# Performance work log

Measured on AMD Instinct MI355X. Metric: run time of the kernel, lower is better.

The kernel has to match this reference:

```python
import jax, jax.numpy as jnp
import numpy as np

N, E, FN, FE, H, L, S = 50000, 800000, 16, 8, 64, 3, 32

def layernorm(h, g, b, eps=1e-5):
    mu = h.mean(-1, keepdims=True)
    var = ((h - mu) ** 2).mean(-1, keepdims=True)
    return (h - mu) / jnp.sqrt(var + eps) * g + b

def setup_inputs() -> dict:
    key = jax.random.key(0)
    ks = iter(jax.random.split(key, 64))
    nrm = lambda shape: jax.random.normal(next(ks), shape, jnp.float32) * 0.05
    inp = {}
    inp['x'] = jax.random.normal(next(ks), (N, FN), jnp.float32)
    inp['edge_index'] = jax.random.randint(next(ks), (2, E), 0, N)
    inp['edge_attr'] = jax.random.normal(next(ks), (E, FE), jnp.float32)
    # node / edge encoders: Linear -> ReLU -> LayerNorm
    inp['Wn'] = nrm((FN, H)); inp['bn'] = jnp.zeros((H,)); inp['gn'] = jnp.ones((H,)); inp['betan'] = jnp.zeros((H,))
    inp['We'] = nrm((FE, H)); inp['be'] = jnp.zeros((H,)); inp['ge'] = jnp.ones((H,)); inp['betae'] = jnp.zeros((H,))
    # EdgeConv MLPs (stacked over layers): Linear(2H,H) -> ReLU -> Linear(H,H)
    inp['Wc1'] = nrm((L, 2 * H, H)); inp['bc1'] = jnp.zeros((L, H))
    inp['Wc2'] = nrm((L, H, H)); inp['bc2'] = jnp.zeros((L, H))
    # GATConv (heads=1): lin weight, att_src, att_dst, bias
    inp['Wg'] = nrm((L, H, H)); inp['att_src'] = nrm((L, H)); inp['att_dst'] = nrm((L, H)); inp['bg'] = jnp.zeros((L, H))
    # q predictor
    inp['Wq1'] = nrm((H, H)); inp['bq1'] = jnp.zeros((H,)); inp['gq'] = jnp.ones((H,)); inp['betaq'] = jnp.zeros((H,))
    inp['Wq2'] = nrm((H, S)); inp['bq2'] = jnp.zeros((S,))
    # value predictor
    inp['Wv1'] = nrm((H, H)); inp['bv1'] = jnp.zeros((H,)); inp['gv'] = jnp.ones((H,)); inp['betav'] = jnp.zeros((H,))
    inp['Wv2'] = nrm((H, 1)); inp['bv2'] = jnp.zeros((1,))
    return inp

def reference(x, edge_index, edge_attr, Wn, bn, gn, betan, We, be, ge, betae,
              Wc1, bc1, Wc2, bc2, Wg, att_src, att_dst, bg,
              Wq1, bq1, gq, betaq, Wq2, bq2, Wv1, bv1, gv, betav, Wv2, bv2):
    n = x.shape[0]
    src, dst = edge_index[0], edge_index[1]  # PyG: row=source(j), col=target(i)
    h = layernorm(jax.nn.relu(x @ Wn + bn), gn, betan)
    _ea = layernorm(jax.nn.relu(edge_attr @ We + be), ge, betae)  # encoded but unused by EdgeConv message (faithful)
    loop = jnp.arange(n)
    gsrc = jnp.concatenate([src, loop])  # GAT adds self-loops
    gdst = jnp.concatenate([dst, loop])
    for l in range(L):
        # EdgeConv: gather x_i (target), x_j (source), concat, MLP, scatter-max at target
        m = jnp.concatenate([h[dst], h[src]], axis=1)  # [E, 2H]
        m = jax.nn.relu(m @ Wc1[l] + bc1[l]) @ Wc2[l] + bc2[l]
        agg = jax.ops.segment_max(m, dst, num_segments=n)
        agg = jnp.where(jnp.isneginf(agg), 0.0, agg)  # PyG scatter-max leaves empty rows at 0
        # GATConv (1 head): alpha = softmax_i(leaky_relu(a_s.xg_j + a_d.xg_i))
        xg = h @ Wg[l]
        a_s = xg @ att_src[l]
        a_d = xg @ att_dst[l]
        e = jax.nn.leaky_relu(a_s[gsrc] + a_d[gdst], 0.2)
        emax = jax.ops.segment_max(e, gdst, num_segments=n)
        w = jnp.exp(e - emax[gdst])
        alpha = w / jax.ops.segment_sum(w, gdst, num_segments=n)[gdst]
        att = jax.ops.segment_sum(xg[gsrc] * alpha[:, None], gdst, num_segments=n) + bg[l]
        h = jax.nn.relu(h + agg + att)
    t = h[0]
    tq = layernorm(jax.nn.relu(t @ Wq1 + bq1), gq, betaq)
    q_values = tq @ Wq2 + bq2
    tv = layernorm(jax.nn.relu(t @ Wv1 + bv1), gv, betav)
    value = tv @ Wv2 + bv2
    return (q_values, value)
```

## Files before the change

### kernel.cpp

```cpp
#include <hip/hip_runtime.h>
#include <math.h>

#define N_NODES 50000
#define N_EDGES 800000
#define FN_DIM 16
#define HD 64
#define T_CAP 8192
#define T2_CAP 512
#define MAXDEG 128

__device__ __forceinline__ float wsum64(float v) {
    #pragma unroll
    for (int o = 1; o < 64; o <<= 1) v += __shfl_xor(v, o);
    return v;
}
__device__ __forceinline__ float wmax64(float v) {
    #pragma unroll
    for (int o = 1; o < 64; o <<= 1) v = fmaxf(v, __shfl_xor(v, o));
    return v;
}
__device__ __forceinline__ float lrelu02(float v) { return v > 0.f ? v : 0.2f * v; }

__global__ void k_mark2(const int* __restrict__ ei, int* need1, int* need2) {
    int e = blockIdx.x * blockDim.x + threadIdx.x;
    if (e == 0) { need1[0] = 1; need2[0] = 1; }
    if (e >= N_EDGES) return;
    if (ei[N_EDGES + e] == 0) { int s = ei[e]; need2[s] = 1; need1[s] = 1; }
}
__global__ void k_mark1(const int* __restrict__ ei, const int* __restrict__ need2, int* need1) {
    int e = blockIdx.x * blockDim.x + threadIdx.x;
    if (e >= N_EDGES) return;
    if (need2[ei[N_EDGES + e]]) need1[ei[e]] = 1;
}
__global__ void k_compact(const int* __restrict__ need1, const int* __restrict__ need2,
                          int* list1, int* list2, int* idx1, int* idx2, int* cnt) {
    int i = blockIdx.x * blockDim.x + threadIdx.x;
    if (i >= N_NODES) return;
    if (need1[i]) { int p = atomicAdd(&cnt[0], 1); if (p < T_CAP)  { list1[p] = i; idx1[i] = p; } }
    if (need2[i]) { int p = atomicAdd(&cnt[1], 1); if (p < T2_CAP) { list2[p] = i; idx2[i] = p; } }
}
__global__ void k_bucket(const int* __restrict__ ei, const int* __restrict__ need1,
                         const int* __restrict__ need2,
                         const int* __restrict__ idx1, const int* __restrict__ idx2,
                         int* eb1, int* deg1, int* eb2, int* deg2, int* eb3, int* deg3) {
    int e = blockIdx.x * blockDim.x + threadIdx.x;
    if (e >= N_EDGES) return;
    int d = ei[N_EDGES + e];
    int s = ei[e];
    if (need1[d]) {
        int t = idx1[d];
        if ((unsigned)t < T_CAP) { int p = atomicAdd(&deg1[t], 1); if (p < MAXDEG) eb1[t * MAXDEG + p] = s; }
    }
    if (need2[d]) {
        int t = idx2[d];
        if ((unsigned)t < T2_CAP) { int p = atomicAdd(&deg2[t], 1); if (p < MAXDEG) eb2[t * MAXDEG + p] = s; }
    }
    if (d == 0) { int p = atomicAdd(deg3, 1); if (p < MAXDEG) eb3[p] = s; }
}

template<int LM>
__device__ __forceinline__ float node_h(int i, int lane,
    const float* __restrict__ x, const float* __restrict__ Wn, const float* __restrict__ bn,
    const float* __restrict__ gn, const float* __restrict__ betan,
    const float* __restrict__ hin) {
    if (LM == 0) {
        float acc = bn[lane];
        #pragma unroll
        for (int k = 0; k < FN_DIM; k++) acc += x[i * FN_DIM + k] * Wn[k * HD + lane];
        float v = fmaxf(acc, 0.f);
        float mu = wsum64(v) * (1.f / 64.f);
        float d = v - mu;
        float var = wsum64(d * d) * (1.f / 64.f);
        return d * rsqrtf(var + 1e-5f) * gn[lane] + betan[lane];
    } else {
        return hin[i * HD + lane];
    }
}

__device__ __forceinline__ void heads_eval(float hv, int lane,
    const float* __restrict__ Wq1, const float* __restrict__ bq1,
    const float* __restrict__ gq, const float* __restrict__ betaq,
    const float* __restrict__ Wq2, const float* __restrict__ bq2,
    const float* __restrict__ Wv1, const float* __restrict__ bv1,
    const float* __restrict__ gv, const float* __restrict__ betav,
    const float* __restrict__ Wv2, const float* __restrict__ bv2,
    float* __restrict__ out) {
    float acc = bq1[lane];
    #pragma unroll 8
    for (int k = 0; k < 64; k++) acc += __shfl(hv, k) * Wq1[k * 64 + lane];
    float r = fmaxf(acc, 0.f);
    float mu = wsum64(r) * (1.f / 64.f);
    float d = r - mu;
    float var = wsum64(d * d) * (1.f / 64.f);
    float tq = d * rsqrtf(var + 1e-5f) * gq[lane] + betaq[lane];
    float accv = bv1[lane];
    #pragma unroll 8
    for (int k = 0; k < 64; k++) accv += __shfl(hv, k) * Wv1[k * 64 + lane];
    float rv = fmaxf(accv, 0.f);
    float muv = wsum64(rv) * (1.f / 64.f);
    float dv = rv - muv;
    float varv = wsum64(dv * dv) * (1.f / 64.f);
    float tv = dv * rsqrtf(varv + 1e-5f) * gv[lane] + betav[lane];
    int s = lane & 31;
    float q = bq2[s];
    #pragma unroll 8
    for (int k = 0; k < 64; k++) q += __shfl(tq, k) * Wq2[k * 32 + s];
    if (lane < 32) out[lane] = q;
    float vsum = wsum64(tv * Wv2[lane]);
    if (lane == 0) out[32] = vsum + bv2[0];
}

template<int LM>
__global__ __launch_bounds__(256) void k_layer(
    const float* __restrict__ x, const float* __restrict__ Wn, const float* __restrict__ bn,
    const float* __restrict__ gn, const float* __restrict__ betan,
    const float* __restrict__ hin,
    const float* __restrict__ Wc1, const float* __restrict__ bc1,
    const float* __restrict__ Wc2, const float* __restrict__ bc2,
    const float* __restrict__ Wg, const float* __restrict__ atts, const float* __restrict__ attd,
    const float* __restrict__ bgv,
    const int* __restrict__ tlist, const int* __restrict__ cntp, int tcap,
    const int* __restrict__ eb, const int* __restrict__ deg,
    float* __restrict__ hout,
    const float* __restrict__ Wq1, const float* __restrict__ bq1,
    const float* __restrict__ gq, const float* __restrict__ betaq,
    const float* __restrict__ Wq2, const float* __restrict__ bq2,
    const float* __restrict__ Wv1, const float* __restrict__ bv1,
    const float* __restrict__ gv, const float* __restrict__ betav,
    const float* __restrict__ Wv2, const float* __restrict__ bv2)
{
    __shared__ float ht[64], ut[64], xgt[64];
    __shared__ float scr[4][4][64];
    __shared__ float xgc[MAXDEG][64];
    __shared__ float ec[MAXDEG];
    __shared__ float redA[4][64], redB[4][64];
    __shared__ float sws[4];
    __shared__ float sA[2];
    __shared__ float sEm;

    int lane = threadIdx.x & 63;
    int wv = threadIdx.x >> 6;
    int ntgt = (LM == 2) ? 1 : min(cntp[0], tcap);

    for (int w = blockIdx.x; w < ntgt; w += gridDim.x) {
        int t = (LM == 2) ? 0 : tlist[w];
        if (wv == 0) {
            float h = node_h<LM>(t, lane, x, Wn, bn, gn, betan, hin);
            ht[lane] = h;
            float u = bc1[lane], xg = 0.f;
            #pragma unroll 4
            for (int k = 0; k < 64; k++) {
                float b = ht[k];
                u  += b * Wc1[k * 64 + lane];
                xg += b * Wg[k * 64 + lane];
            }
            ut[lane] = u; xgt[lane] = xg;
            float a_st = wsum64(xg * atts[lane]);
            float a_dt = wsum64(xg * attd[lane]);
            if (lane == 0) { sA[0] = a_st; sA[1] = a_dt; }
        }
        __syncthreads();
        int dg = deg[(LM == 2) ? 0 : w]; if (dg > MAXDEG) dg = MAXDEG;
        float a_dt = sA[1];
        float aggw = -INFINITY;

        for (int base = wv * 4; base < dg; base += 16) {
            int ne = dg - base; if (ne > 4) ne = 4;
            #pragma unroll
            for (int e = 0; e < 4; e++) {
                if (e < ne) {
                    int s = eb[w * MAXDEG + base + e];
                    scr[wv][e][lane] = node_h<LM>(s, lane, x, Wn, bn, gn, betan, hin);
                }
            }
            float v[4] = {0.f, 0.f, 0.f, 0.f};
            float g[4] = {0.f, 0.f, 0.f, 0.f};
            #pragma unroll 4
            for (int k = 0; k < 64; k++) {
                float wc = Wc1[(64 + k) * 64 + lane];
                float wg = Wg[k * 64 + lane];
                #pragma unroll
                for (int e = 0; e < 4; e++) {
                    float b = scr[wv][e][k];
                    v[e] += b * wc;
                    g[e] += b * wg;
                }
            }
            float ut_l = ut[lane];
            #pragma unroll
            for (int e = 0; e < 4; e++) scr[wv][e][lane] = fmaxf(ut_l + v[e], 0.f);
            float m[4];
            #pragma unroll
            for (int e = 0; e < 4; e++) m[e] = bc2[lane];
            #pragma unroll 4
            for (int k = 0; k < 64; k++) {
                float wc2v = Wc2[k * 64 + lane];
                #pragma unroll
                for (int e = 0; e < 4; e++) m[e] += scr[wv][e][k] * wc2v;
            }
            #pragma unroll
            for (int e = 0; e < 4; e++) {
                if (e < ne) {
                    aggw = fmaxf(aggw, m[e]);
                    int j = base + e;
                    xgc[j][lane] = g[e];
                    float a_ss = wsum64(g[e] * atts[lane]);
                    if (lane == 0) ec[j] = lrelu02(a_ss + a_dt);
                }
            }
        }
        redA[wv][lane] = aggw;
        __syncthreads();

        if (wv == 0) {
            float es = lrelu02(sA[0] + sA[1]);
            float mm = es;
            for (int j = lane; j < dg; j += 64) mm = fmaxf(mm, ec[j]);
            mm = wmax64(mm);
            if (lane == 0) sEm = mm;
        }
        __syncthreads();
        float em = sEm;
        float attv = 0.f, wsv = 0.f;
        for (int j = wv; j < dg; j += 4) {
            float wj = expf(ec[j] - em);
            attv += wj * xgc[j][lane];
            wsv += wj;
        }
        redB[wv][lane] = attv;
        if (lane == 0) sws[wv] = wsv;
        __syncthreads();

        if (wv == 0) {
            float agg = fmaxf(fmaxf(redA[0][lane], redA[1][lane]),
                              fmaxf(redA[2][lane], redA[3][lane]));
            if (dg == 0) agg = 0.f;
            float es = lrelu02(sA[0] + sA[1]);
            float wself = expf(es - em);
            float att = redB[0][lane] + redB[1][lane] + redB[2][lane] + redB[3][lane]
                      + wself * xgt[lane];
            float wsum = sws[0] + sws[1] + sws[2] + sws[3] + wself;
            float hv = fmaxf(ht[lane] + agg + att / wsum + bgv[lane], 0.f);
            if (LM == 2) {
                heads_eval(hv, lane, Wq1, bq1, gq, betaq, Wq2, bq2,
                           Wv1, bv1, gv, betav, Wv2, bv2, hout);
            } else {
                hout[t * HD + lane] = hv;
            }
        }
        __syncthreads();
    }
}

extern "C" void kernel_launch(void* const* d_in, const int* in_sizes, int n_in,
                              void* d_out, int out_size, void* d_ws, size_t ws_size,
                              hipStream_t stream) {
    const float* x        = (const float*)d_in[0];
    const int*   ei       = (const int*)d_in[1];
    const float* Wn       = (const float*)d_in[3];
    const float* bn       = (const float*)d_in[4];
    const float* gn       = (const float*)d_in[5];
    const float* betan    = (const float*)d_in[6];
    const float* Wc1      = (const float*)d_in[11];
    const float* bc1      = (const float*)d_in[12];
    const float* Wc2      = (const float*)d_in[13];
    const float* bc2      = (const float*)d_in[14];
    const float* Wg       = (const float*)d_in[15];
    const float* att_src  = (const float*)d_in[16];
    const float* att_dst  = (const float*)d_in[17];
    const float* bg       = (const float*)d_in[18];
    const float* Wq1      = (const float*)d_in[19];
    const float* bq1      = (const float*)d_in[20];
    const float* gq       = (const float*)d_in[21];
    const float* betaq    = (const float*)d_in[22];
    const float* Wq2      = (const float*)d_in[23];
    const float* bq2      = (const float*)d_in[24];
    const float* Wv1      = (const float*)d_in[25];
    const float* bv1      = (const float*)d_in[26];
    const float* gv       = (const float*)d_in[27];
    const float* betav    = (const float*)d_in[28];
    const float* Wv2      = (const float*)d_in[29];
    const float* bv2      = (const float*)d_in[30];

    float* hB   = (float*)d_ws;
    float* hA   = hB + (size_t)N_NODES * HD;
    int* need1  = (int*)(hA + (size_t)N_NODES * HD);
    int* need2  = need1 + N_NODES;
    int* deg1   = need2 + N_NODES;
    int* deg2   = deg1 + T_CAP;
    int* deg3   = deg2 + T2_CAP;
    int* cnt    = deg3 + 4;
    int* idx1   = cnt + 8;
    int* idx2   = idx1 + N_NODES;
    int* list1  = idx2 + N_NODES;
    int* list2  = list1 + T_CAP;
    int* eb1    = list2 + T2_CAP;
    int* eb2    = eb1 + (size_t)T_CAP * MAXDEG;
    int* eb3    = eb2 + (size_t)T2_CAP * MAXDEG;

    size_t zero_ints = (size_t)2 * N_NODES + T_CAP + T2_CAP + 12;
    hipMemsetAsync(need1, 0, zero_ints * sizeof(int), stream);

    const int EB = (N_EDGES + 255) / 256;
    const int NB = (N_NODES + 255) / 256;

    k_mark2<<<EB, 256, 0, stream>>>(ei, need1, need2);
    k_mark1<<<EB, 256, 0, stream>>>(ei, need2, need1);
    k_compact<<<NB, 256, 0, stream>>>(need1, need2, list1, list2, idx1, idx2, cnt);
    k_bucket<<<EB, 256, 0, stream>>>(ei, need1, need2, idx1, idx2,
                                     eb1, deg1, eb2, deg2, eb3, deg3);

    k_layer<0><<<512, 256, 0, stream>>>(
        x, Wn, bn, gn, betan, (const float*)nullptr,
        Wc1 + 0 * 2 * HD * HD, bc1 + 0 * HD, Wc2 + 0 * HD * HD, bc2 + 0 * HD,
        Wg + 0 * HD * HD, att_src + 0 * HD, att_dst + 0 * HD, bg + 0 * HD,
        list1, cnt + 0, T_CAP, eb1, deg1, hB,
        Wq1, bq1, gq, betaq, Wq2, bq2, Wv1, bv1, gv, betav, Wv2, bv2);

    k_layer<1><<<64, 256, 0, stream>>>(
        x, Wn, bn, gn, betan, hB,
        Wc1 + 1 * 2 * HD * HD, bc1 + 1 * HD, Wc2 + 1 * HD * HD, bc2 + 1 * HD,
        Wg + 1 * HD * HD, att_src + 1 * HD, att_dst + 1 * HD, bg + 1 * HD,
        list2, cnt + 1, T2_CAP, eb2, deg2, hA,
        Wq1, bq1, gq, betaq, Wq2, bq2, Wv1, bv1, gv, betav, Wv2, bv2);

    k_layer<2><<<1, 256, 0, stream>>>(
        x, Wn, bn, gn, betan, hA,
        Wc1 + 2 * 2 * HD * HD, bc1 + 2 * HD, Wc2 + 2 * HD * HD, bc2 + 2 * HD,
        Wg + 2 * HD * HD, att_src + 2 * HD, att_dst + 2 * HD, bg + 2 * HD,
        (const int*)nullptr, cnt + 1, 1, eb3, deg3, (float*)d_out,
        Wq1, bq1, gq, betaq, Wq2, bq2, Wv1, bv1, gv, betav, Wv2, bv2);
}
```

Baseline: 98.36 us.

## Fuse all stages into one cooperative persistent kernel with online softmax

Replaces the memset, four graph-preprocessing kernels and three per-layer kernels with a single cooperative kernel that uses grid-wide syncs between phases. Layer weights are staged in shared memory. The GAT projection is folded so attention logits come from h·(Wg·att) vectors. Attention aggregates raw h with an online softmax and applies Wg once afterwards, and edge arrays are read with int4 loads. It also lowers the target-list caps (T_CAP 8192→1024, T2_CAP 64), which risks truncating the needed node sets, and relies on grid sync overhead being smaller than launch overhead.

```diff
diff --git a/kernel.cpp b/kernel.cpp
--- a/kernel.cpp
+++ b/kernel.cpp
@@ -1,333 +1,329 @@
 #include <hip/hip_runtime.h>
+#include <hip/hip_cooperative_groups.h>
 #include <math.h>
+
+namespace cg = cooperative_groups;
 
 #define N_NODES 50000
 #define N_EDGES 800000
 #define FN_DIM 16
 #define HD 64
-#define T_CAP 8192
-#define T2_CAP 512
+#define T_CAP 1024
+#define T2_CAP 64
 #define MAXDEG 128
+#define NBLK 256
+#define NTHR 256
+
+struct KP {
+  const float *x; const int *ei;
+  const float *Wn,*bn,*gn,*betan;
+  const float *Wc1,*bc1,*Wc2,*bc2;
+  const float *Wg,*att_s,*att_d,*bg;
+  const float *Wq1,*bq1,*gq,*betaq,*Wq2,*bq2;
+  const float *Wv1,*bv1,*gv,*betav,*Wv2,*bv2;
+  float *out;
+  float *hB,*hA,*pvec;
+  int *need1,*need2,*deg1,*deg2,*deg3,*cnt,*idx1,*idx2,*list1,*list2,*eb1,*eb2,*eb3;
+  int zero4;
+};
 
 __device__ __forceinline__ float wsum64(float v) {
     #pragma unroll
     for (int o = 1; o < 64; o <<= 1) v += __shfl_xor(v, o);
     return v;
 }
-__device__ __forceinline__ float wmax64(float v) {
-    #pragma unroll
-    for (int o = 1; o < 64; o <<= 1) v = fmaxf(v, __shfl_xor(v, o));
-    return v;
-}
 __device__ __forceinline__ float lrelu02(float v) { return v > 0.f ? v : 0.2f * v; }
 
-__global__ void k_mark2(const int* __restrict__ ei, int* need1, int* need2) {
-    int e = blockIdx.x * blockDim.x + threadIdx.x;
-    if (e == 0) { need1[0] = 1; need2[0] = 1; }
-    if (e >= N_EDGES) return;
-    if (ei[N_EDGES + e] == 0) { int s = ei[e]; need2[s] = 1; need1[s] = 1; }
-}
-__global__ void k_mark1(const int* __restrict__ ei, const int* __restrict__ need2, int* need1) {
-    int e = blockIdx.x * blockDim.x + threadIdx.x;
-    if (e >= N_EDGES) return;
-    if (need2[ei[N_EDGES + e]]) need1[ei[e]] = 1;
-}
-__global__ void k_compact(const int* __restrict__ need1, const int* __restrict__ need2,
-                          int* list1, int* list2, int* idx1, int* idx2, int* cnt) {
-    int i = blockIdx.x * blockDim.x + threadIdx.x;
-    if (i >= N_NODES) return;
-    if (need1[i]) { int p = atomicAdd(&cnt[0], 1); if (p < T_CAP)  { list1[p] = i; idx1[i] = p; } }
-    if (need2[i]) { int p = atomicAdd(&cnt[1], 1); if (p < T2_CAP) { list2[p] = i; idx2[i] = p; } }
-}
-__global__ void k_bucket(const int* __restrict__ ei, const int* __restrict__ need1,
-                         const int* __restrict__ need2,
-                         const int* __restrict__ idx1, const int* __restrict__ idx2,
-                         int* eb1, int* deg1, int* eb2, int* deg2, int* eb3, int* deg3) {
-    int e = blockIdx.x * blockDim.x + threadIdx.x;
-    if (e >= N_EDGES) return;
-    int d = ei[N_EDGES + e];
-    int s = ei[e];
-    if (need1[d]) {
-        int t = idx1[d];
-        if ((unsigned)t < T_CAP) { int p = atomicAdd(&deg1[t], 1); if (p < MAXDEG) eb1[t * MAXDEG + p] = s; }
-    }
-    if (need2[d]) {
-        int t = idx2[d];
-        if ((unsigned)t < T2_CAP) { int p = atomicAdd(&deg2[t], 1); if (p < MAXDEG) eb2[t * MAXDEG + p] = s; }
-    }
-    if (d == 0) { int p = atomicAdd(deg3, 1); if (p < MAXDEG) eb3[p] = s; }
-}
-
-template<int LM>
-__device__ __forceinline__ float node_h(int i, int lane,
-    const float* __restrict__ x, const float* __restrict__ Wn, const float* __restrict__ bn,
-    const float* __restrict__ gn, const float* __restrict__ betan,
-    const float* __restrict__ hin) {
-    if (LM == 0) {
-        float acc = bn[lane];
+__global__ __launch_bounds__(NTHR, 1) void k_all(KP p) {
+    cg::grid_group gg = cg::this_grid();
+    __shared__ float wA[HD * HD];
+    __shared__ float wB[HD * HD];
+    __shared__ float wC[HD * HD];
+    __shared__ float wG[HD * HD];
+    __shared__ float wN[FN_DIM * HD];
+    __shared__ float sv[8 * HD];
+    __shared__ float redA[4][HD], redH[4][HD];
+    __shared__ float sM[4], sW[4], sHbar[HD];
+
+    const int tid = threadIdx.x, lane = tid & 63, wv = tid >> 6;
+    const int bid = blockIdx.x;
+    const int gt = bid * NTHR + tid, gsz = NBLK * NTHR;
+
+    int4* zb = (int4*)p.need1;
+    for (int i = gt; i < p.zero4; i += gsz) zb[i] = make_int4(0, 0, 0, 0);
+    gg.sync();
+
+    const int4* d4p = (const int4*)(p.ei + N_EDGES);
+    const int4* s4p = (const int4*)p.ei;
+    if (gt == 0) { p.need1[0] = 1; p.need2[0] = 1; }
+    for (int i = gt; i < N_EDGES / 4; i += gsz) {
+        int4 d4 = d4p[i], s4 = s4p[i];
+        if (d4.x == 0) { p.need2[s4.x] = 1; p.need1[s4.x] = 1; }
+        if (d4.y == 0) { p.need2[s4.y] = 1; p.need1[s4.y] = 1; }
+        if (d4.z == 0) { p.need2[s4.z] = 1; p.need1[s4.z] = 1; }
+        if (d4.w == 0) { p.need2[s4.w] = 1; p.need1[s4.w] = 1; }
+    }
+    gg.sync();
+
+    for (int i = gt; i < N_EDGES / 4; i += gsz) {
+        int4 d4 = d4p[i], s4 = s4p[i];
+        if (p.need2[d4.x]) p.need1[s4.x] = 1;
+        if (p.need2[d4.y]) p.need1[s4.y] = 1;
+        if (p.need2[d4.z]) p.need1[s4.z] = 1;
+        if (p.need2[d4.w]) p.need1[s4.w] = 1;
+    }
+    gg.sync();
+
+    for (int i = gt; i < N_NODES; i += gsz) {
+        if (p.need1[i]) { int q = atomicAdd(&p.cnt[0], 1); if (q < T_CAP)  { p.list1[q] = i; p.idx1[i] = q; } }
+        if (p.need2[i]) { int q = atomicAdd(&p.cnt[1], 1); if (q < T2_CAP) { p.list2[q] = i; p.idx2[i] = q; } }
+    }
+    if (bid < 6 && wv == 0) {
+        int l = bid >> 1, which = bid & 1;
+        const float* att = (which ? p.att_d : p.att_s) + l * HD;
+        float av = att[lane];
+        const float* wg = p.Wg + l * HD * HD + lane * HD;
+        float acc = 0.f;
+        #pragma unroll 8
+        for (int c = 0; c < HD; c++) acc += wg[c] * __shfl(av, c);
+        p.pvec[l * 2 * HD + which * HD + lane] = acc;
+    }
+    gg.sync();
+
+    for (int i = gt; i < N_EDGES / 4; i += gsz) {
+        int4 d4 = d4p[i], s4 = s4p[i];
+        int dd[4] = {d4.x, d4.y, d4.z, d4.w};
+        int ss[4] = {s4.x, s4.y, s4.z, s4.w};
         #pragma unroll
-        for (int k = 0; k < FN_DIM; k++) acc += x[i * FN_DIM + k] * Wn[k * HD + lane];
-        float v = fmaxf(acc, 0.f);
-        float mu = wsum64(v) * (1.f / 64.f);
-        float d = v - mu;
-        float var = wsum64(d * d) * (1.f / 64.f);
-        return d * rsqrtf(var + 1e-5f) * gn[lane] + betan[lane];
-    } else {
-        return hin[i * HD + lane];
-    }
-}
-
-__device__ __forceinline__ void heads_eval(float hv, int lane,
-    const float* __restrict__ Wq1, const float* __restrict__ bq1,
-    const float* __restrict__ gq, const float* __restrict__ betaq,
-    const float* __restrict__ Wq2, const float* __restrict__ bq2,
-    const float* __restrict__ Wv1, const float* __restrict__ bv1,
-    const float* __restrict__ gv, const float* __restrict__ betav,
-    const float* __restrict__ Wv2, const float* __restrict__ bv2,
-    float* __restrict__ out) {
-    float acc = bq1[lane];
-    #pragma unroll 8
-    for (int k = 0; k < 64; k++) acc += __shfl(hv, k) * Wq1[k * 64 + lane];
-    float r = fmaxf(acc, 0.f);
-    float mu = wsum64(r) * (1.f / 64.f);
-    float d = r - mu;
-    float var = wsum64(d * d) * (1.f / 64.f);
-    float tq = d * rsqrtf(var + 1e-5f) * gq[lane] + betaq[lane];
-    float accv = bv1[lane];
-    #pragma unroll 8
-    for (int k = 0; k < 64; k++) accv += __shfl(hv, k) * Wv1[k * 64 + lane];
-    float rv = fmaxf(accv, 0.f);
-    float muv = wsum64(rv) * (1.f / 64.f);
-    float dv = rv - muv;
-    float varv = wsum64(dv * dv) * (1.f / 64.f);
-    float tv = dv * rsqrtf(varv + 1e-5f) * gv[lane] + betav[lane];
-    int s = lane & 31;
-    float q = bq2[s];
-    #pragma unroll 8
-    for (int k = 0; k < 64; k++) q += __shfl(tq, k) * Wq2[k * 32 + s];
-    if (lane < 32) out[lane] = q;
-    float vsum = wsum64(tv * Wv2[lane]);
-    if (lane == 0) out[32] = vsum + bv2[0];
-}
-
-template<int LM>
-__global__ __launch_bounds__(256) void k_layer(
-    const float* __restrict__ x, const float* __restrict__ Wn, const float* __restrict__ bn,
-    const float* __restrict__ gn, const float* __restrict__ betan,
-    const float* __restrict__ hin,
-    const float* __restrict__ Wc1, const float* __restrict__ bc1,
-    const float* __restrict__ Wc2, const float* __restrict__ bc2,
-    const float* __restrict__ Wg, const float* __restrict__ atts, const float* __restrict__ attd,
-    const float* __restrict__ bgv,
-    const int* __restrict__ tlist, const int* __restrict__ cntp, int tcap,
-    const int* __restrict__ eb, const int* __restrict__ deg,
-    float* __restrict__ hout,
-    const float* __restrict__ Wq1, const float* __restrict__ bq1,
-    const float* __restrict__ gq, const float* __restrict__ betaq,
-    const float* __restrict__ Wq2, const float* __restrict__ bq2,
-    const float* __restrict__ Wv1, const float* __restrict__ bv1,
-    const float* __restrict__ gv, const float* __restrict__ betav,
-    const float* __restrict__ Wv2, const float* __restrict__ bv2)
-{
-    __shared__ float ht[64], ut[64], xgt[64];
-    __shared__ float scr[4][4][64];
-    __shared__ float xgc[MAXDEG][64];
-    __shared__ float ec[MAXDEG];
-    __shared__ float redA[4][64], redB[4][64];
-    __shared__ float sws[4];
-    __shared__ float sA[2];
-    __shared__ float sEm;
-
-    int lane = threadIdx.x & 63;
-    int wv = threadIdx.x >> 6;
-    int ntgt = (LM == 2) ? 1 : min(cntp[0], tcap);
-
-    for (int w = blockIdx.x; w < ntgt; w += gridDim.x) {
-        int t = (LM == 2) ? 0 : tlist[w];
+        for (int c = 0; c < 4; c++) {
+            int d = dd[c], s = ss[c];
+            if (p.need1[d]) {
+                int t = p.idx1[d];
+                if ((unsigned)t < T_CAP) { int q = atomicAdd(&p.deg1[t], 1); if (q < MAXDEG) p.eb1[t * MAXDEG + q] = s; }
+            }
+            if (p.need2[d]) {
+                int t = p.idx2[d];
+                if ((unsigned)t < T2_CAP) { int q = atomicAdd(&p.deg2[t], 1); if (q < MAXDEG) p.eb2[t * MAXDEG + q] = s; }
+            }
+            if (d == 0) { int q = atomicAdd(p.deg3, 1); if (q < MAXDEG) p.eb3[q] = s; }
+        }
+    }
+    gg.sync();
+
+    for (int l = 0; l < 3; l++) {
+        const float* Wc1l = p.Wc1 + l * 2 * HD * HD;
+        for (int i = tid; i < HD * HD / 4; i += NTHR) {
+            ((float4*)wA)[i] = ((const float4*)Wc1l)[i];
+            ((float4*)wB)[i] = ((const float4*)(Wc1l + HD * HD))[i];
+            ((float4*)wC)[i] = ((const float4*)(p.Wc2 + l * HD * HD))[i];
+            ((float4*)wG)[i] = ((const float4*)(p.Wg + l * HD * HD))[i];
+        }
+        if (l == 0)
+            for (int i = tid; i < FN_DIM * HD / 4; i += NTHR)
+                ((float4*)wN)[i] = ((const float4*)p.Wn)[i];
+        if (tid < HD) {
+            sv[0 * HD + tid] = p.bc1[l * HD + tid];
+            sv[1 * HD + tid] = p.bc2[l * HD + tid];
+            sv[2 * HD + tid] = p.bg[l * HD + tid];
+            sv[3 * HD + tid] = p.pvec[l * 2 * HD + tid];
+            sv[4 * HD + tid] = p.pvec[l * 2 * HD + HD + tid];
+            sv[5 * HD + tid] = p.bn[tid];
+            sv[6 * HD + tid] = p.gn[tid];
+            sv[7 * HD + tid] = p.betan[tid];
+        }
+        __syncthreads();
+
+        int ntgt = (l == 0) ? min(p.cnt[0], T_CAP) : (l == 1) ? min(p.cnt[1], T2_CAP) : 1;
+        const int* tl  = (l == 0) ? p.list1 : p.list2;
+        const int* ebp = (l == 0) ? p.eb1 : (l == 1) ? p.eb2 : p.eb3;
+        const int* dgp = (l == 0) ? p.deg1 : (l == 1) ? p.deg2 : p.deg3;
+        const float* hin = (l == 1) ? p.hB : p.hA;
+        float* hout = (l == 0) ? p.hB : p.hA;
+
+        for (int w = bid; w < ntgt; w += NBLK) {
+            int t = (l == 2) ? 0 : tl[w];
+            int dg = dgp[(l == 2) ? 0 : w]; if (dg > MAXDEG) dg = MAXDEG;
+            const int* row = ebp + (size_t)((l == 2) ? 0 : w) * MAXDEG;
+
+            float hval;
+            if (l == 0) {
+                float xv = p.x[t * FN_DIM + (lane & 15)];
+                float acc = sv[5 * HD + lane];
+                #pragma unroll
+                for (int k = 0; k < FN_DIM; k++) acc += __shfl(xv, k) * wN[k * HD + lane];
+                float vv = fmaxf(acc, 0.f);
+                float mu = wsum64(vv) * (1.f / 64.f);
+                float d2 = vv - mu;
+                float var = wsum64(d2 * d2) * (1.f / 64.f);
+                hval = d2 * rsqrtf(var + 1e-5f) * sv[6 * HD + lane] + sv[7 * HD + lane];
+            } else hval = hin[(size_t)t * HD + lane];
+
+            float a_st = wsum64(hval * sv[3 * HD + lane]);
+            float a_dt = wsum64(hval * sv[4 * HD + lane]);
+            float es = lrelu02(a_st + a_dt);
+
+            float uval = sv[0 * HD + lane];
+            #pragma unroll 8
+            for (int k = 0; k < HD; k++) uval += __shfl(hval, k) * wA[k * HD + lane];
+
+            float aggw = -INFINITY, mrun = -INFINITY, wpart = 0.f, hw = 0.f;
+            for (int j = wv; j < dg; j += 4) {
+                int s = row[j];
+                float hs;
+                if (l == 0) {
+                    float xv = p.x[s * FN_DIM + (lane & 15)];
+                    float acc = sv[5 * HD + lane];
+                    #pragma unroll
+                    for (int k = 0; k < FN_DIM; k++) acc += __shfl(xv, k) * wN[k * HD + lane];
+                    float vv = fmaxf(acc, 0.f);
+                    float mu = wsum64(vv) * (1.f / 64.f);
+                    float d2 = vv - mu;
+                    float var = wsum64(d2 * d2) * (1.f / 64.f);
+                    hs = d2 * rsqrtf(var + 1e-5f) * sv[6 * HD + lane] + sv[7 * HD + lane];
+                } else hs = hin[(size_t)s * HD + lane];
+
+                float logit = lrelu02(wsum64(hs * sv[3 * HD + lane]) + a_dt);
+                float v = 0.f;
+                #pragma unroll 8
+                for (int k = 0; k < HD; k++) v += __shfl(hs, k) * wB[k * HD + lane];
+                float hid = fmaxf(uval + v, 0.f);
+                float m = sv[1 * HD + lane];
+                #pragma unroll 8
+                for (int k = 0; k < HD; k++) m += __shfl(hid, k) * wC[k * HD + lane];
+                aggw = fmaxf(aggw, m);
+                if (logit > mrun) { float sc = expf(mrun - logit); hw *= sc; wpart *= sc; mrun = logit; }
+                float we = expf(logit - mrun);
+                hw += we * hs; wpart += we;
+            }
+            redA[wv][lane] = aggw;
+            redH[wv][lane] = hw;
+            if (lane == 0) { sM[wv] = mrun; sW[wv] = wpart; }
+            __syncthreads();
+
+            if (wv == 0) {
+                float M = es;
+                #pragma unroll
+                for (int q = 0; q < 4; q++) M = fmaxf(M, sM[q]);
+                float den = expf(es - M);
+                float num = den * hval;
+                #pragma unroll
+                for (int q = 0; q < 4; q++) {
+                    float sc = (sM[q] == -INFINITY) ? 0.f : expf(sM[q] - M);
+                    num += sc * redH[q][lane];
+                    den += sc * sW[q];
+                }
+                float hbar = num / den;
+                float att = sv[2 * HD + lane];
+                #pragma unroll 8
+                for (int k = 0; k < HD; k++) att += __shfl(hbar, k) * wG[k * HD + lane];
+                float agg = fmaxf(fmaxf(redA[0][lane], redA[1][lane]),
+                                  fmaxf(redA[2][lane], redA[3][lane]));
+                if (dg == 0) agg = 0.f;
+                float hv = fmaxf(hval + agg + att, 0.f);
+                if (l < 2) hout[(size_t)t * HD + lane] = hv;
+                else sHbar[lane] = hv;
+            }
+            __syncthreads();
+        }
+        if (l < 2) gg.sync();
+    }
+
+    if (bid == 0) {
+        for (int i = tid; i < HD * HD / 4; i += NTHR) {
+            ((float4*)wA)[i] = ((const float4*)p.Wq1)[i];
+            ((float4*)wB)[i] = ((const float4*)p.Wv1)[i];
+        }
+        for (int i = tid; i < HD * 32 / 4; i += NTHR)
+            ((float4*)wC)[i] = ((const float4*)p.Wq2)[i];
+        if (tid < HD) {
+            sv[0 * HD + tid] = p.bq1[tid]; sv[1 * HD + tid] = p.gq[tid];
+            sv[2 * HD + tid] = p.betaq[tid];
+            sv[3 * HD + tid] = p.bv1[tid]; sv[4 * HD + tid] = p.gv[tid];
+            sv[5 * HD + tid] = p.betav[tid];
+            sv[6 * HD + tid] = p.Wv2[tid];
+        }
+        if (tid < 32) sv[7 * HD + tid] = p.bq2[tid];
+        __syncthreads();
+        float hvv = sHbar[lane];
         if (wv == 0) {
-            float h = node_h<LM>(t, lane, x, Wn, bn, gn, betan, hin);
-            ht[lane] = h;
-            float u = bc1[lane], xg = 0.f;
-            #pragma unroll 4
-            for (int k = 0; k < 64; k++) {
-                float b = ht[k];
-                u  += b * Wc1[k * 64 + lane];
-                xg += b * Wg[k * 64 + lane];
-            }
-            ut[lane] = u; xgt[lane] = xg;
-            float a_st = wsum64(xg * atts[lane]);
-            float a_dt = wsum64(xg * attd[lane]);
-            if (lane == 0) { sA[0] = a_st; sA[1] = a_dt; }
-        }
-        __syncthreads();
-        int dg = deg[(LM == 2) ? 0 : w]; if (dg > MAXDEG) dg = MAXDEG;
-        float a_dt = sA[1];
-        float aggw = -INFINITY;
-
-        for (int base = wv * 4; base < dg; base += 16) {
-            int ne = dg - base; if (ne > 4) ne = 4;
-            #pragma unroll
-            for (int e = 0; e < 4; e++) {
-                if (e < ne) {
-                    int s = eb[w * MAXDEG + base + e];
-                    scr[wv][e][lane] = node_h<LM>(s, lane, x, Wn, bn, gn, betan, hin);
-                }
-            }
-            float v[4] = {0.f, 0.f, 0.f, 0.f};
-            float g[4] = {0.f, 0.f, 0.f, 0.f};
-            #pragma unroll 4
-            for (int k = 0; k < 64; k++) {
-                float wc = Wc1[(64 + k) * 64 + lane];
-                float wg = Wg[k * 64 + lane];
-                #pragma unroll
-                for (int e = 0; e < 4; e++) {
-                    float b = scr[wv][e][k];
-                    v[e] += b * wc;
-                    g[e] += b * wg;
-                }
-            }
-            float ut_l = ut[lane];
-            #pragma unroll
-            for (int e = 0; e < 4; e++) scr[wv][e][lane] = fmaxf(ut_l + v[e], 0.f);
-            float m[4];
-            #pragma unroll
-            for (int e = 0; e < 4; e++) m[e] = bc2[lane];
-            #pragma unroll 4
-            for (int k = 0; k < 64; k++) {
-                float wc2v = Wc2[k * 64 + lane];
-                #pragma unroll
-                for (int e = 0; e < 4; e++) m[e] += scr[wv][e][k] * wc2v;
-            }
-            #pragma unroll
-            for (int e = 0; e < 4; e++) {
-                if (e < ne) {
-                    aggw = fmaxf(aggw, m[e]);
-                    int j = base + e;
-                    xgc[j][lane] = g[e];
-                    float a_ss = wsum64(g[e] * atts[lane]);
-                    if (lane == 0) ec[j] = lrelu02(a_ss + a_dt);
-                }
-            }
-        }
-        redA[wv][lane] = aggw;
-        __syncthreads();
-
-        if (wv == 0) {
-            float es = lrelu02(sA[0] + sA[1]);
-            float mm = es;
-            for (int j = lane; j < dg; j += 64) mm = fmaxf(mm, ec[j]);
-            mm = wmax64(mm);
-            if (lane == 0) sEm = mm;
-        }
-        __syncthreads();
-        float em = sEm;
-        float attv = 0.f, wsv = 0.f;
-        for (int j = wv; j < dg; j += 4) {
-            float wj = expf(ec[j] - em);
-            attv += wj * xgc[j][lane];
-            wsv += wj;
-        }
-        redB[wv][lane] = attv;
-        if (lane == 0) sws[wv] = wsv;
-        __syncthreads();
-
-        if (wv == 0) {
-            float agg = fmaxf(fmaxf(redA[0][lane], redA[1][lane]),
-                              fmaxf(redA[2][lane], redA[3][lane]));
-            if (dg == 0) agg = 0.f;
-            float es = lrelu02(sA[0] + sA[1]);
-            float wself = expf(es - em);
-            float att = redB[0][lane] + redB[1][lane] + redB[2][lane] + redB[3][lane]
-                      + wself * xgt[lane];
-            float wsum = sws[0] + sws[1] + sws[2] + sws[3] + wself;
-            float hv = fmaxf(ht[lane] + agg + att / wsum + bgv[lane], 0.f);
-            if (LM == 2) {
-                heads_eval(hv, lane, Wq1, bq1, gq, betaq, Wq2, bq2,
-                           Wv1, bv1, gv, betav, Wv2, bv2, hout);
-            } else {
-                hout[t * HD + lane] = hv;
-            }
-        }
-        __syncthreads();
+            float acc = sv[0 * HD + lane];
+            #pragma unroll 8
+            for (int k = 0; k < HD; k++) acc += __shfl(hvv, k) * wA[k * HD + lane];
+            float r = fmaxf(acc, 0.f);
+            float mu = wsum64(r) * (1.f / 64.f);
+            float d2 = r - mu;
+            float var = wsum64(d2 * d2) * (1.f / 64.f);
+            float tq = d2 * rsqrtf(var + 1e-5f) * sv[1 * HD + lane] + sv[2 * HD + lane];
+            int s2 = lane & 31;
+            float q = sv[7 * HD + s2];
+            #pragma unroll 8
+            for (int k = 0; k < HD; k++) q += __shfl(tq, k) * wC[k * 32 + s2];
+            if (lane < 32) p.out[lane] = q;
+        } else if (wv == 1) {
+            float accv = sv[3 * HD + lane];
+            #pragma unroll 8
+            for (int k = 0; k < HD; k++) accv += __shfl(hvv, k) * wB[k * HD + lane];
+            float rv = fmaxf(accv, 0.f);
+            float muv = wsum64(rv) * (1.f / 64.f);
+            float dv = rv - muv;
+            float varv = wsum64(dv * dv) * (1.f / 64.f);
+            float tv = dv * rsqrtf(varv + 1e-5f) * sv[4 * HD + lane] + sv[5 * HD + lane];
+            float vs = wsum64(tv * sv[6 * HD + lane]);
+            if (lane == 0) p.out[32] = vs + p.bv2[0];
+        }
     }
 }
 
 extern "C" void kernel_launch(void* const* d_in, const int* in_sizes, int n_in,
                               void* d_out, int out_size, void* d_ws, size_t ws_size,
                               hipStream_t stream) {
-    const float* x        = (const float*)d_in[0];
-    const int*   ei       = (const int*)d_in[1];
-    const float* Wn       = (const float*)d_in[3];
-    const float* bn       = (const float*)d_in[4];
-    const float* gn       = (const float*)d_in[5];
-    const float* betan    = (const float*)d_in[6];
-    const float* Wc1      = (const float*)d_in[11];
-    const float* bc1      = (const float*)d_in[12];
-    const float* Wc2      = (const float*)d_in[13];
-    const float* bc2      = (const float*)d_in[14];
-    const float* Wg       = (const float*)d_in[15];
-    const float* att_src  = (const float*)d_in[16];
-    const float* att_dst  = (const float*)d_in[17];
-    const float* bg       = (const float*)d_in[18];
-    const float* Wq1      = (const float*)d_in[19];
-    const float* bq1      = (const float*)d_in[20];
-    const float* gq       = (const float*)d_in[21];
-    const float* betaq    = (const float*)d_in[22];
-    const float* Wq2      = (const float*)d_in[23];
-    const float* bq2      = (const float*)d_in[24];
-    const float* Wv1      = (const float*)d_in[25];
-    const float* bv1      = (const float*)d_in[26];
-    const float* gv       = (const float*)d_in[27];
-    const float* betav    = (const float*)d_in[28];
-    const float* Wv2      = (const float*)d_in[29];
-    const float* bv2      = (const float*)d_in[30];
-
-    float* hB   = (float*)d_ws;
-    float* hA   = hB + (size_t)N_NODES * HD;
-    int* need1  = (int*)(hA + (size_t)N_NODES * HD);
-    int* need2  = need1 + N_NODES;
-    int* deg1   = need2 + N_NODES;
-    int* deg2   = deg1 + T_CAP;
-    int* deg3   = deg2 + T2_CAP;
-    int* cnt    = deg3 + 4;
-    int* idx1   = cnt + 8;
-    int* idx2   = idx1 + N_NODES;
-    int* list1  = idx2 + N_NODES;
-    int* list2  = list1 + T_CAP;
-    int* eb1    = list2 + T2_CAP;
-    int* eb2    = eb1 + (size_t)T_CAP * MAXDEG;
-    int* eb3    = eb2 + (size_t)T2_CAP * MAXDEG;
-
-    size_t zero_ints = (size_t)2 * N_NODES + T_CAP + T2_CAP + 12;
-    hipMemsetAsync(need1, 0, zero_ints * sizeof(int), stream);
-
-    const int EB = (N_EDGES + 255) / 256;
-    const int NB = (N_NODES + 255) / 256;
-
-    k_mark2<<<EB, 256, 0, stream>>>(ei, need1, need2);
-    k_mark1<<<EB, 256, 0, stream>>>(ei, need2, need1);
-    k_compact<<<NB, 256, 0, stream>>>(need1, need2, list1, list2, idx1, idx2, cnt);
-    k_bucket<<<EB, 256, 0, stream>>>(ei, need1, need2, idx1, idx2,
-                                     eb1, deg1, eb2, deg2, eb3, deg3);
-
-    k_layer<0><<<512, 256, 0, stream>>>(
-        x, Wn, bn, gn, betan, (const float*)nullptr,
-        Wc1 + 0 * 2 * HD * HD, bc1 + 0 * HD, Wc2 + 0 * HD * HD, bc2 + 0 * HD,
-        Wg + 0 * HD * HD, att_src + 0 * HD, att_dst + 0 * HD, bg + 0 * HD,
-        list1, cnt + 0, T_CAP, eb1, deg1, hB,
-        Wq1, bq1, gq, betaq, Wq2, bq2, Wv1, bv1, gv, betav, Wv2, bv2);
-
-    k_layer<1><<<64, 256, 0, stream>>>(
-        x, Wn, bn, gn, betan, hB,
-        Wc1 + 1 * 2 * HD * HD, bc1 + 1 * HD, Wc2 + 1 * HD * HD, bc2 + 1 * HD,
-        Wg + 1 * HD * HD, att_src + 1 * HD, att_dst + 1 * HD, bg + 1 * HD,
-        list2, cnt + 1, T2_CAP, eb2, deg2, hA,
-        Wq1, bq1, gq, betaq, Wq2, bq2, Wv1, bv1, gv, betav, Wv2, bv2);
-
-    k_layer<2><<<1, 256, 0, stream>>>(
-        x, Wn, bn, gn, betan, hA,
-        Wc1 + 2 * 2 * HD * HD, bc1 + 2 * HD, Wc2 + 2 * HD * HD, bc2 + 2 * HD,
-        Wg + 2 * HD * HD, att_src + 2 * HD, att_dst + 2 * HD, bg + 2 * HD,
-        (const int*)nullptr, cnt + 1, 1, eb3, deg3, (float*)d_out,
-        Wq1, bq1, gq, betaq, Wq2, bq2, Wv1, bv1, gv, betav, Wv2, bv2);
+    KP p;
+    p.x      = (const float*)d_in[0];
+    p.ei     = (const int*)d_in[1];
+    p.Wn     = (const float*)d_in[3];
+    p.bn     = (const float*)d_in[4];
+    p.gn     = (const float*)d_in[5];
+    p.betan  = (const float*)d_in[6];
+    p.Wc1    = (const float*)d_in[11];
+    p.bc1    = (const float*)d_in[12];
+    p.Wc2    = (const float*)d_in[13];
+    p.bc2    = (const float*)d_in[14];
+    p.Wg     = (const float*)d_in[15];
+    p.att_s  = (const float*)d_in[16];
+    p.att_d  = (const float*)d_in[17];
+    p.bg     = (const float*)d_in[18];
+    p.Wq1    = (const float*)d_in[19];
+    p.bq1    = (const float*)d_in[20];
+    p.gq     = (const float*)d_in[21];
+    p.betaq  = (const float*)d_in[22];
+    p.Wq2    = (const float*)d_in[23];
+    p.bq2    = (const float*)d_in[24];
+    p.Wv1    = (const float*)d_in[25];
+    p.bv1    = (const float*)d_in[26];
+    p.gv     = (const float*)d_in[27];
+    p.betav  = (const float*)d_in[28];
+    p.Wv2    = (const float*)d_in[29];
+    p.bv2    = (const float*)d_in[30];
+    p.out    = (float*)d_out;
+
+    p.hB    = (float*)d_ws;
+    p.hA    = p.hB + (size_t)N_NODES * HD;
+    p.need1 = (int*)(p.hA + (size_t)N_NODES * HD);
+    p.need2 = p.need1 + N_NODES;
+    p.deg1  = p.need2 + N_NODES;
+    p.deg2  = p.deg1 + T_CAP;
+    p.deg3  = p.deg2 + T2_CAP;
+    p.cnt   = p.deg3 + 4;
+    p.idx1  = p.cnt + 8;
+    p.idx2  = p.idx1 + N_NODES;
+    p.list1 = p.idx2 + N_NODES;
+    p.list2 = p.list1 + T_CAP;
+    p.eb1   = p.list2 + T2_CAP;
+    p.eb2   = p.eb1 + (size_t)T_CAP * MAXDEG;
+    p.eb3   = p.eb2 + (size_t)T2_CAP * MAXDEG;
+    p.pvec  = (float*)(p.eb3 + MAXDEG);
+    p.zero4 = (2 * N_NODES + T_CAP + T2_CAP + 12) / 4;
+
+    void* kargs[] = { (void*)&p };
+    hipLaunchCooperativeKernel((void*)k_all, dim3(NBLK), dim3(NTHR), kargs, 0, stream);
 }
```

After: 291.6 us. 196% more time.
